# Kernel optimization log

Hardware: AMD Instinct MI355X
Metric: run time of the kernel (lower is better)

Reference implementation:

```python
import math
import jax, jax.numpy as jnp
import numpy as np

T, D, H = 2048, 1024, 16
DH = D // H
DFF = 4 * D
EPS = 1e-5


def gelu(x):
    c = math.sqrt(2.0 / math.pi)
    return 0.5 * x * (1.0 + jnp.tanh(c * (x + 0.044715 * jnp.power(x, 3))))


def layer_norm(x, w, b):
    mu = jnp.mean(x, axis=-1, keepdims=True)
    var = jnp.var(x, axis=-1, keepdims=True)
    return (x - mu) / jnp.sqrt(var + EPS) * w + b


def setup_inputs() -> dict:
    key = jax.random.key(0)
    ks = jax.random.split(key, 8)
    s = lambda fan_in: 1.0 / math.sqrt(fan_in)
    return {
        "x": jax.random.normal(ks[0], (T, D), jnp.float32),
        "w_kqv": jax.random.uniform(ks[1], (3 * D, D), jnp.float32, -s(D), s(D)),
        "b_kqv": jnp.zeros((3 * D,), jnp.float32),
        "w_o": jax.random.uniform(ks[2], (D, D), jnp.float32, -s(D), s(D)),
        "b_o": jnp.zeros((D,), jnp.float32),
        "ln1_w": jnp.ones((D,), jnp.float32),
        "ln1_b": jnp.zeros((D,), jnp.float32),
        "ln2_w": jnp.ones((D,), jnp.float32),
        "ln2_b": jnp.zeros((D,), jnp.float32),
        "w_up": jax.random.uniform(ks[3], (DFF, D), jnp.float32, -s(D), s(D)),
        "b_up": jnp.zeros((DFF,), jnp.float32),
        "w_down": jax.random.uniform(ks[4], (D, DFF), jnp.float32, -s(DFF), s(DFF)),
        "b_down": jnp.zeros((D,), jnp.float32),
    }


def _block(x, w_kqv, b_kqv, w_o, b_o, ln1_w, ln1_b, ln2_w, ln2_b,
           w_up, b_up, w_down, b_down):
    t = x.shape[0]
    # --- causal attention ---
    h = layer_norm(x, ln1_w, ln1_b)
    kqv = h @ w_kqv.T + b_kqv                      # [t, 3D]
    k, q, v = jnp.split(kqv, 3, axis=-1)
    # rearrange 't (d h) -> h t d' : head index is the FAST axis (as in source)
    to_heads = lambda m: m.reshape(t, DH, H).transpose(2, 0, 1)  # [H, t, DH]
    k, q, v = to_heads(k), to_heads(q), to_heads(v)
    # NOTE: source divides by sqrt(1/d) == multiplies by sqrt(d_head)
    logits = jnp.einsum('hqd,hkd->hqk', q, k) * math.sqrt(DH)
    mask = jnp.tril(jnp.ones((t, t), dtype=bool))
    logits = jnp.where(mask, logits, -jnp.inf)
    attn_w = jax.nn.softmax(logits, axis=-1)       # [H, t, t]
    hv = jnp.einsum('hqK,hKd->hqd', attn_w, v)     # [H, t, DH]
    # rearrange 'h q d -> q (h d)' : head index is the SLOW axis (as in source)
    hv = hv.transpose(1, 0, 2).reshape(t, D)
    x = x + (hv @ w_o.T + b_o)
    # --- MLP ---
    h2 = layer_norm(x, ln2_w, ln2_b)
    z = gelu(h2 @ w_up.T + b_up) @ w_down.T + b_down
    return x + z


def reference(x, w_kqv, b_kqv, w_o, b_o, ln1_w, ln1_b, ln2_w, ln2_b,
              w_up, b_up, w_down, b_down):
    return _block(x, w_kqv, b_kqv, w_o, b_o, ln1_w, ln1_b, ln2_w, ln2_b,
                  w_up, b_up, w_down, b_down)
```

## Files before the change

kernel.cpp:

```cpp
#include <hip/hip_runtime.h>
#include <math.h>

#define TT 2048
#define DD 1024
#define NH 16
#define DHD 64
#define DFF 4096

typedef __attribute__((ext_vector_type(8))) short short8;
typedef __attribute__((ext_vector_type(4))) float f32x4;

#define MFMA16(a, b, c) __builtin_amdgcn_mfma_f32_16x16x32_bf16(a, b, c, 0, 0, 0)
#define GLDS16(gp, lp) __builtin_amdgcn_global_load_lds( \
    (const __attribute__((address_space(1))) void*)(gp), \
    (__attribute__((address_space(3))) void*)(lp), 16, 0, 0)

static __device__ __forceinline__ unsigned short f2b(float f) {
  unsigned u = __builtin_bit_cast(unsigned, f);
  u = u + 0x7fffu + ((u >> 16) & 1u);
  return (unsigned short)(u >> 16);
}
static __device__ __forceinline__ float b2f(unsigned short b) {
  return __builtin_bit_cast(float, (unsigned)b << 16);
}

__global__ __launch_bounds__(256) void f2b_kernel(const float* __restrict__ in,
    unsigned short* __restrict__ out, int n4) {
  int i = blockIdx.x * 256 + threadIdx.x;
  if (i >= n4) return;
  float4 v = ((const float4*)in)[i];
  ushort4 o;
  o.x = f2b(v.x); o.y = f2b(v.y); o.z = f2b(v.z); o.w = f2b(v.w);
  ((ushort4*)out)[i] = o;
}

__global__ __launch_bounds__(256) void ln_kernel(const float* __restrict__ x,
    const float* __restrict__ w, const float* __restrict__ b,
    unsigned short* __restrict__ out) {
  int row = blockIdx.x;
  const float4* xr = (const float4*)(x + (size_t)row * DD);
  float4 v = xr[threadIdx.x];
  float s  = v.x + v.y + v.z + v.w;
  float ss = v.x * v.x + v.y * v.y + v.z * v.z + v.w * v.w;
  for (int o = 32; o > 0; o >>= 1) {
    s  += __shfl_down(s, o);
    ss += __shfl_down(ss, o);
  }
  __shared__ float red[10];
  int lane = threadIdx.x & 63, wv = threadIdx.x >> 6;
  if (lane == 0) { red[wv] = s; red[4 + wv] = ss; }
  __syncthreads();
  if (threadIdx.x == 0) {
    float S  = red[0] + red[1] + red[2] + red[3];
    float SS = red[4] + red[5] + red[6] + red[7];
    float mu  = S * (1.0f / DD);
    float var = SS * (1.0f / DD) - mu * mu;
    red[8] = mu;
    red[9] = rsqrtf(var + 1e-5f);
  }
  __syncthreads();
  float mu = red[8], inv = red[9];
  float4 wv4 = ((const float4*)w)[threadIdx.x];
  float4 bv4 = ((const float4*)b)[threadIdx.x];
  ushort4 o4;
  o4.x = f2b((v.x - mu) * inv * wv4.x + bv4.x);
  o4.y = f2b((v.y - mu) * inv * wv4.y + bv4.y);
  o4.z = f2b((v.z - mu) * inv * wv4.z + bv4.z);
  o4.w = f2b((v.w - mu) * inv * wv4.w + bv4.w);
  ((ushort4*)(out + (size_t)row * DD))[threadIdx.x] = o4;
}

template<int FUSE_GELU, int OUT_BF16, int HAS_RESID, int PARTIAL>
__global__ __launch_bounds__(256) void gemm2(
    const unsigned short* __restrict__ A,
    const unsigned short* __restrict__ Bw,
    const float* __restrict__ bias,
    const float* __restrict__ resid,
    void* __restrict__ Cout,
    int M, int N, int K, int KS) {
  __shared__ char lds[65536];
  const int tid = threadIdx.x;
  const int w = tid >> 6, l = tid & 63;
  const int l15 = l & 15, lhi = l >> 4;
  const int row0 = blockIdx.y * 128, col0 = blockIdx.x * 128;
  const int kbeg = blockIdx.z * KS;
  const int wm = (w >> 1) * 64, wn = (w & 1) * 64;

  f32x4 acc[4][4] = {};

  const int lrow = l >> 3;
  const int cb = ((l & 7) * 16) ^ (lrow << 4);
  const size_t rs8 = (size_t)K * 16;
  const char* aS = (const char*)A + ((size_t)(row0 + w * 32 + lrow) * K + kbeg) * 2 + cb;
  const char* bS = (const char*)Bw + ((size_t)(col0 + w * 32 + lrow) * K + kbeg) * 2 + cb;
  char* aD = lds + w * 4096;
  char* bD = lds + 16384 + w * 4096;

  const int NT = KS >> 6;

#pragma unroll
  for (int i = 0; i < 4; ++i) {
    GLDS16(aS + i * rs8, aD + i * 1024);
    GLDS16(bS + i * rs8, bD + i * 1024);
  }
  aS += 128; bS += 128;
  __syncthreads();

  int cur = 0;
  for (int t = 0; t < NT; ++t) {
    if (t + 1 < NT) {
      char* aDn = aD + (cur ^ 1) * 32768;
      char* bDn = bD + (cur ^ 1) * 32768;
#pragma unroll
      for (int i = 0; i < 4; ++i) {
        GLDS16(aS + i * rs8, aDn + i * 1024);
        GLDS16(bS + i * rs8, bDn + i * 1024);
      }
      aS += 128; bS += 128;
    }
    const char* Ab = lds + cur * 32768;
    const char* Bb = Ab + 16384;
    const int swz = (l15 & 7) << 4;
#pragma unroll
    for (int kk = 0; kk < 2; ++kk) {
      short8 af[4], bf[4];
#pragma unroll
      for (int mi = 0; mi < 4; ++mi)
        af[mi] = *(const short8*)(Ab + (wm + mi * 16 + l15) * 128 + ((kk * 64 + lhi * 16) ^ swz));
#pragma unroll
      for (int ni = 0; ni < 4; ++ni)
        bf[ni] = *(const short8*)(Bb + (wn + ni * 16 + l15) * 128 + ((kk * 64 + lhi * 16) ^ swz));
#pragma unroll
      for (int mi = 0; mi < 4; ++mi)
#pragma unroll
        for (int ni = 0; ni < 4; ++ni)
          acc[mi][ni] = MFMA16(af[mi], bf[ni], acc[mi][ni]);
    }
    __syncthreads();
    cur ^= 1;
  }

  if (PARTIAL) {
    float* Cp = (float*)Cout + (size_t)blockIdx.z * M * N;
#pragma unroll
    for (int mi = 0; mi < 4; ++mi)
#pragma unroll
      for (int r = 0; r < 4; ++r) {
        size_t row = (size_t)(row0 + wm + mi * 16 + lhi * 4 + r);
#pragma unroll
        for (int ni = 0; ni < 4; ++ni)
          Cp[row * N + col0 + wn + ni * 16 + l15] = acc[mi][ni][r];
      }
    return;
  }

#pragma unroll
  for (int mi = 0; mi < 4; ++mi) {
#pragma unroll
    for (int r = 0; r < 4; ++r) {
      size_t row = (size_t)(row0 + wm + mi * 16 + lhi * 4 + r);
#pragma unroll
      for (int ni = 0; ni < 4; ++ni) {
        int col = col0 + wn + ni * 16 + l15;
        float v = acc[mi][ni][r] + bias[col];
        if (FUSE_GELU) {
          float u = v;
          v = 0.5f * u * (1.0f + tanhf(0.7978845608028654f * (u + 0.044715f * u * u * u)));
        }
        if (HAS_RESID) v += resid[row * N + col];
        if (OUT_BF16) ((unsigned short*)Cout)[row * N + col] = f2b(v);
        else          ((float*)Cout)[row * N + col] = v;
      }
    }
  }
}

__global__ __launch_bounds__(256) void reduce_down(const float* __restrict__ p,
    const float* __restrict__ bias, const float* __restrict__ resid,
    float* __restrict__ out) {
  int i = blockIdx.x * 256 + threadIdx.x;
  float4 a = ((const float4*)p)[i];
  float4 b = ((const float4*)(p + (size_t)TT * DD))[i];
  float4 r = ((const float4*)resid)[i];
  float4 bb = ((const float4*)bias)[i & (DD / 4 - 1)];
  float4 o;
  o.x = a.x + b.x + r.x + bb.x;
  o.y = a.y + b.y + r.y + bb.y;
  o.z = a.z + b.z + r.z + bb.z;
  o.w = a.w + b.w + r.w + bb.w;
  ((float4*)out)[i] = o;
}

__global__ __launch_bounds__(256) void gather_qkv(const unsigned short* __restrict__ kqv,
    unsigned short* __restrict__ Q, unsigned short* __restrict__ K,
    unsigned short* __restrict__ V) {
  int idx = blockIdx.x * 256 + threadIdx.x;
  int d = idx & 63;
  int t = (idx >> 6) & (TT - 1);
  int h = idx >> 17;
  int col = d * NH + h;
  const unsigned short* rowp = kqv + (size_t)t * (3 * DD);
  K[idx] = rowp[col];
  Q[idx] = f2b(b2f(rowp[DD + col]) * 8.0f);
  V[idx] = rowp[2 * DD + col];
}

__global__ __launch_bounds__(256) void attn_mfma(
    const unsigned short* __restrict__ Q,
    const unsigned short* __restrict__ K,
    const unsigned short* __restrict__ V,
    unsigned short* __restrict__ hv) {
  const int h = blockIdx.y;
  const int qb = gridDim.x - 1 - blockIdx.x;
  const int q0 = qb * 64;
  const int tid = threadIdx.x;
  const int w = tid >> 6, l = tid & 63;
  const int l15 = l & 15, lhi = l >> 4;

  __shared__ unsigned short Ks[64 * 64];
  __shared__ unsigned short Vt[64 * 64];
  __shared__ unsigned short Ps[4][16 * 64];

  const unsigned short* Kh = K + (size_t)h * TT * DHD;
  const unsigned short* Vh = V + (size_t)h * TT * DHD;

  const unsigned short* Qbase = Q + ((size_t)h * TT + q0 + w * 16 + l15) * DHD;
  short8 qf0 = *(const short8*)(Qbase + lhi * 8);
  short8 qf1 = *(const short8*)(Qbase + 32 + lhi * 8);

  f32x4 oacc[4] = {};
  float m[4], lsum[4];
#pragma unroll
  for (int r = 0; r < 4; ++r) { m[r] = -INFINITY; lsum[r] = 0.0f; }

  const int krow = w * 16 + (l >> 3);
  const int kswz = (krow & 7) << 4;
  const int kcolb = ((l & 7) * 16) ^ kswz;
  char* kL = (char*)Ks + w * 2048;

  for (int kt = 0; kt <= qb; ++kt) {
    const int k0 = kt * 64;
    __syncthreads();

    GLDS16((const char*)(Kh + (size_t)(k0 + krow) * DHD) + kcolb, kL);
    GLDS16((const char*)(Kh + (size_t)(k0 + krow + 8) * DHD) + kcolb, kL + 1024);

    {
      const char* vS = (const char*)(Vh + (size_t)(k0 + l) * DHD) + w * 16;
      short8 v0 = *(const short8*)vS;
      short8 v1 = *(const short8*)(vS + 64);
#pragma unroll
      for (int j = 0; j < 8; ++j) {
        int d = w * 8 + j;
        *(unsigned short*)((char*)Vt + d * 128 + ((2 * l) ^ (j << 4))) =
            (unsigned short)v0[j];
        *(unsigned short*)((char*)Vt + (d + 32) * 128 + ((2 * l) ^ (j << 4))) =
            (unsigned short)v1[j];
      }
    }
    __syncthreads();

    f32x4 sacc[4] = {};
    {
      const char* kr = (const char*)Ks;
      int swz = (l15 & 7) << 4;
#pragma unroll
      for (int nt = 0; nt < 4; ++nt) {
        const char* rowp = kr + (nt * 16 + l15) * 128;
        short8 kb0 = *(const short8*)(rowp + ((lhi * 16) ^ swz));
        short8 kb1 = *(const short8*)(rowp + ((64 + lhi * 16) ^ swz));
        sacc[nt] = MFMA16(qf0, kb0, sacc[nt]);
        sacc[nt] = MFMA16(qf1, kb1, sacc[nt]);
      }
    }

    if (kt == qb) {
      const int qrow = w * 16 + lhi * 4;
#pragma unroll
      for (int nt = 0; nt < 4; ++nt)
#pragma unroll
        for (int r = 0; r < 4; ++r)
          if (nt * 16 + l15 > qrow + r) sacc[nt][r] = -INFINITY;
    }

    float mnew[4], al[4];
#pragma unroll
    for (int r = 0; r < 4; ++r) {
      float t = fmaxf(fmaxf(sacc[0][r], sacc[1][r]), fmaxf(sacc[2][r], sacc[3][r]));
      t = fmaxf(t, __shfl_xor(t, 1));
      t = fmaxf(t, __shfl_xor(t, 2));
      t = fmaxf(t, __shfl_xor(t, 4));
      t = fmaxf(t, __shfl_xor(t, 8));
      mnew[r] = fmaxf(m[r], t);
      al[r] = __expf(m[r] - mnew[r]);
      m[r] = mnew[r];
    }
#pragma unroll
    for (int r = 0; r < 4; ++r) {
      float s = 0.0f;
#pragma unroll
      for (int nt = 0; nt < 4; ++nt) {
        float p = __expf(sacc[nt][r] - mnew[r]);
        sacc[nt][r] = p;
        s += p;
      }
      s += __shfl_xor(s, 1);
      s += __shfl_xor(s, 2);
      s += __shfl_xor(s, 4);
      s += __shfl_xor(s, 8);
      lsum[r] = lsum[r] * al[r] + s;
#pragma unroll
      for (int dt = 0; dt < 4; ++dt) oacc[dt][r] *= al[r];
    }

    {
      char* pw = (char*)Ps[w];
#pragma unroll
      for (int r = 0; r < 4; ++r) {
        int prow = lhi * 4 + r;
        char* pp = pw + prow * 128;
        int swz = (prow & 7) << 4;
#pragma unroll
        for (int nt = 0; nt < 4; ++nt)
          *(unsigned short*)(pp + ((nt * 32 + l15 * 2) ^ swz)) = f2b(sacc[nt][r]);
      }
    }

    {
      const char* pr = (const char*)Ps[w] + l15 * 128;
      int pswz = (l15 & 7) << 4;
      short8 pa0 = *(const short8*)(pr + ((lhi * 16) ^ pswz));
      short8 pa1 = *(const short8*)(pr + ((64 + lhi * 16) ^ pswz));
      int vswz = (l15 & 7) << 4;
#pragma unroll
      for (int dt = 0; dt < 4; ++dt) {
        const char* vr = (const char*)Vt + (dt * 16 + l15) * 128;
        short8 vb0 = *(const short8*)(vr + ((lhi * 16) ^ vswz));
        short8 vb1 = *(const short8*)(vr + ((64 + lhi * 16) ^ vswz));
        oacc[dt] = MFMA16(pa0, vb0, oacc[dt]);
        oacc[dt] = MFMA16(pa1, vb1, oacc[dt]);
      }
    }
  }

#pragma unroll
  for (int r = 0; r < 4; ++r) {
    float inv = 1.0f / lsum[r];
    size_t orow = (size_t)(q0 + w * 16 + lhi * 4 + r) * DD + h * 64;
#pragma unroll
    for (int dt = 0; dt < 4; ++dt)
      hv[orow + dt * 16 + l15] = f2b(oacc[dt][r] * inv);
  }
}

extern "C" void kernel_launch(void* const* d_in, const int* in_sizes, int n_in,
                              void* d_out, int out_size, void* d_ws, size_t ws_size,
                              hipStream_t stream) {
  const float* x     = (const float*)d_in[0];
  const float* w_kqv = (const float*)d_in[1];
  const float* b_kqv = (const float*)d_in[2];
  const float* w_o   = (const float*)d_in[3];
  const float* b_o   = (const float*)d_in[4];
  const float* ln1_w = (const float*)d_in[5];
  const float* ln1_b = (const float*)d_in[6];
  const float* ln2_w = (const float*)d_in[7];
  const float* ln2_b = (const float*)d_in[8];
  const float* w_up  = (const float*)d_in[9];
  const float* b_up  = (const float*)d_in[10];
  const float* w_dn  = (const float*)d_in[11];
  const float* b_dn  = (const float*)d_in[12];
  float* out = (float*)d_out;

  char* W = (char*)d_ws;
  unsigned short* wkqv_b = (unsigned short*)(W);
  unsigned short* wo_b   = (unsigned short*)(W + 6291456);
  unsigned short* wup_b  = (unsigned short*)(W + 8388608);
  unsigned short* wdn_b  = (unsigned short*)(W + 16777216);
  unsigned short* h_b    = (unsigned short*)(W + 25165824);
  unsigned short* kqz    = (unsigned short*)(W + 29360128);
  unsigned short* Qg     = (unsigned short*)(W + 46137344);
  unsigned short* Kg     = (unsigned short*)(W + 50331648);
  unsigned short* Vg     = (unsigned short*)(W + 54525952);
  unsigned short* hv_b   = (unsigned short*)(W + 58720256);
  float*          x2     = (float*)(W + 62914560);
  float*          part   = (float*)(W + 46137344);

  f2b_kernel<<<(3 * DD * DD / 4 + 255) / 256, 256, 0, stream>>>(w_kqv, wkqv_b, 3 * DD * DD / 4);
  f2b_kernel<<<(DD * DD / 4 + 255) / 256, 256, 0, stream>>>(w_o, wo_b, DD * DD / 4);
  f2b_kernel<<<(DFF * DD / 4 + 255) / 256, 256, 0, stream>>>(w_up, wup_b, DFF * DD / 4);
  f2b_kernel<<<(DD * DFF / 4 + 255) / 256, 256, 0, stream>>>(w_dn, wdn_b, DD * DFF / 4);

  ln_kernel<<<TT, 256, 0, stream>>>(x, ln1_w, ln1_b, h_b);
  gemm2<0, 1, 0, 0><<<dim3(3 * DD / 128, TT / 128, 1), 256, 0, stream>>>(
      h_b, wkqv_b, b_kqv, nullptr, kqz, TT, 3 * DD, DD, DD);
  gather_qkv<<<(NH * TT * DHD) / 256, 256, 0, stream>>>(kqz, Qg, Kg, Vg);
  attn_mfma<<<dim3(TT / 64, NH), 256, 0, stream>>>(Qg, Kg, Vg, hv_b);
  gemm2<0, 0, 1, 0><<<dim3(DD / 128, TT / 128, 1), 256, 0, stream>>>(
      hv_b, wo_b, b_o, x, x2, TT, DD, DD, DD);
  ln_kernel<<<TT, 256, 0, stream>>>(x2, ln2_w, ln2_b, h_b);
  gemm2<1, 1, 0, 0><<<dim3(DFF / 128, TT / 128, 1), 256, 0, stream>>>(
      h_b, wup_b, b_up, nullptr, kqz, TT, DFF, DD, DD);
  gemm2<0, 0, 0, 1><<<dim3(DD / 128, TT / 128, 2), 256, 0, stream>>>(
      kqz, wdn_b, nullptr, nullptr, part, TT, DD, DFF, DFF / 2);
  reduce_down<<<TT * DD / 4 / 256, 256, 0, stream>>>(part, b_dn, x2, out);
}
```

Baseline: 211.3 us.

## Double-buffer attention K/V tiles with pre-transposed V and merged weight casts

Attention now double-buffers K and V tiles in LDS with async global-to-LDS loads, prefetching the next tile while computing the current one. To allow this, V is pre-transposed into a head-major [d, t] layout by a new transpose kernel instead of being transposed through LDS scatter inside the loop. The score MFMA operands are swapped so each lane owns one query row, which simplifies the softmax reductions. The four weight-cast launches are merged into one. The cost is an extra transpose launch and a larger LDS footprint, which may lower occupancy.

Result: faster. 179.8 us (-14.9%).

```diff
diff --git a/kernel.cpp b/kernel.cpp
--- a/kernel.cpp
+++ b/kernel.cpp
@@ -24,11 +24,16 @@
   return __builtin_bit_cast(float, (unsigned)b << 16);
 }
 
-__global__ __launch_bounds__(256) void f2b_kernel(const float* __restrict__ in,
-    unsigned short* __restrict__ out, int n4) {
+__global__ __launch_bounds__(256) void f2b4_kernel(const float* __restrict__ s0,
+    const float* __restrict__ s1, const float* __restrict__ s2,
+    const float* __restrict__ s3, unsigned short* __restrict__ out) {
   int i = blockIdx.x * 256 + threadIdx.x;
-  if (i >= n4) return;
-  float4 v = ((const float4*)in)[i];
+  const float* s; int off;
+  if (i < 786432)       { s = s0; off = 0; }
+  else if (i < 1048576) { s = s1; off = 786432; }
+  else if (i < 2097152) { s = s2; off = 1048576; }
+  else                  { s = s3; off = 2097152; }
+  float4 v = ((const float4*)s)[i - off];
   ushort4 o;
   o.x = f2b(v.x); o.y = f2b(v.y); o.z = f2b(v.z); o.w = f2b(v.w);
   ((ushort4*)out)[i] = o;
@@ -192,8 +197,7 @@
 }
 
 __global__ __launch_bounds__(256) void gather_qkv(const unsigned short* __restrict__ kqv,
-    unsigned short* __restrict__ Q, unsigned short* __restrict__ K,
-    unsigned short* __restrict__ V) {
+    unsigned short* __restrict__ Q, unsigned short* __restrict__ K) {
   int idx = blockIdx.x * 256 + threadIdx.x;
   int d = idx & 63;
   int t = (idx >> 6) & (TT - 1);
@@ -202,13 +206,28 @@
   const unsigned short* rowp = kqv + (size_t)t * (3 * DD);
   K[idx] = rowp[col];
   Q[idx] = f2b(b2f(rowp[DD + col]) * 8.0f);
-  V[idx] = rowp[2 * DD + col];
+}
+
+__global__ __launch_bounds__(256) void transpose_v(const unsigned short* __restrict__ kqv,
+    unsigned short* __restrict__ Vt) {
+  const int h = blockIdx.y;
+  const int t0 = blockIdx.x * 64;
+  __shared__ unsigned short Vs[64][65];
+  for (int idx = threadIdx.x; idx < 4096; idx += 256) {
+    int t = idx >> 6, d = idx & 63;
+    Vs[t][d] = kqv[(size_t)(t0 + t) * (3 * DD) + 2 * DD + d * NH + h];
+  }
+  __syncthreads();
+  for (int idx = threadIdx.x; idx < 4096; idx += 256) {
+    int d = idx >> 6, t = idx & 63;
+    Vt[(size_t)(h * DHD + d) * TT + t0 + t] = Vs[t][d];
+  }
 }
 
 __global__ __launch_bounds__(256) void attn_mfma(
     const unsigned short* __restrict__ Q,
     const unsigned short* __restrict__ K,
-    const unsigned short* __restrict__ V,
+    const unsigned short* __restrict__ Vt,
     unsigned short* __restrict__ hv) {
   const int h = blockIdx.y;
   const int qb = gridDim.x - 1 - blockIdx.x;
@@ -217,139 +236,134 @@
   const int w = tid >> 6, l = tid & 63;
   const int l15 = l & 15, lhi = l >> 4;
 
-  __shared__ unsigned short Ks[64 * 64];
-  __shared__ unsigned short Vt[64 * 64];
-  __shared__ unsigned short Ps[4][16 * 64];
-
-  const unsigned short* Kh = K + (size_t)h * TT * DHD;
-  const unsigned short* Vh = V + (size_t)h * TT * DHD;
+  __shared__ char lds[40960];
+  char* Ps = lds + 32768 + w * 2048;
+
+  const char* KhB = (const char*)(K + (size_t)h * TT * DHD);
+  const char* VhB = (const char*)(Vt + (size_t)h * DHD * TT);
 
   const unsigned short* Qbase = Q + ((size_t)h * TT + q0 + w * 16 + l15) * DHD;
   short8 qf0 = *(const short8*)(Qbase + lhi * 8);
   short8 qf1 = *(const short8*)(Qbase + 32 + lhi * 8);
 
   f32x4 oacc[4] = {};
-  float m[4], lsum[4];
-#pragma unroll
-  for (int r = 0; r < 4; ++r) { m[r] = -INFINITY; lsum[r] = 0.0f; }
-
-  const int krow = w * 16 + (l >> 3);
-  const int kswz = (krow & 7) << 4;
-  const int kcolb = ((l & 7) * 16) ^ kswz;
-  char* kL = (char*)Ks + w * 2048;
+  float m = -1e30f, lsum = 0.0f;
+
+  const int lrow = l >> 3;
+  const int colb = ((l & 7) * 16) ^ (lrow << 4);
+  const int srow = w * 16 + lrow;
+  const int swz = (l15 & 7) << 4;
+
+  auto stage = [&](int k0n, char* buf) {
+    const char* ks = KhB + (size_t)(k0n + srow) * 128 + colb;
+    GLDS16(ks, buf + w * 2048);
+    GLDS16(ks + 8 * 128, buf + w * 2048 + 1024);
+    const char* vs = VhB + (size_t)srow * (TT * 2) + (size_t)k0n * 2 + colb;
+    GLDS16(vs, buf + 8192 + w * 2048);
+    GLDS16(vs + 8 * (TT * 2), buf + 8192 + w * 2048 + 1024);
+  };
+
+  stage(0, lds);
+  __syncthreads();
+  int cur = 0;
 
   for (int kt = 0; kt <= qb; ++kt) {
-    const int k0 = kt * 64;
+    if (kt < qb) stage((kt + 1) * 64, lds + (cur ^ 1) * 16384);
+
+    const char* Kb = lds + cur * 16384;
+    const char* Vb = Kb + 8192;
+
+    f32x4 sacc[4] = {};
+    __builtin_amdgcn_s_setprio(1);
+#pragma unroll
+    for (int nt = 0; nt < 4; ++nt) {
+      const char* rp = Kb + (nt * 16 + l15) * 128;
+      short8 kb0 = *(const short8*)(rp + ((lhi * 16) ^ swz));
+      short8 kb1 = *(const short8*)(rp + ((64 + lhi * 16) ^ swz));
+      sacc[nt] = MFMA16(kb0, qf0, sacc[nt]);
+      sacc[nt] = MFMA16(kb1, qf1, sacc[nt]);
+    }
+    __builtin_amdgcn_s_setprio(0);
+
+    if (kt == qb) {
+      const int qloc = w * 16 + l15;
+#pragma unroll
+      for (int nt = 0; nt < 4; ++nt)
+#pragma unroll
+        for (int r = 0; r < 4; ++r)
+          if (nt * 16 + lhi * 4 + r > qloc) sacc[nt][r] = -1e30f;
+    }
+
+    float tmax = -1e30f;
+#pragma unroll
+    for (int nt = 0; nt < 4; ++nt)
+#pragma unroll
+      for (int r = 0; r < 4; ++r) tmax = fmaxf(tmax, sacc[nt][r]);
+    tmax = fmaxf(tmax, __shfl_xor(tmax, 16));
+    tmax = fmaxf(tmax, __shfl_xor(tmax, 32));
+    float mnew = fmaxf(m, tmax);
+    float al = __expf(m - mnew);
+    m = mnew;
+    float ssum = 0.0f;
+#pragma unroll
+    for (int nt = 0; nt < 4; ++nt)
+#pragma unroll
+      for (int r = 0; r < 4; ++r) {
+        float p = __expf(sacc[nt][r] - mnew);
+        sacc[nt][r] = p;
+        ssum += p;
+      }
+    ssum += __shfl_xor(ssum, 16);
+    ssum += __shfl_xor(ssum, 32);
+    lsum = lsum * al + ssum;
+
+    {
+      char* pp = Ps + l15 * 128;
+#pragma unroll
+      for (int nt = 0; nt < 4; ++nt) {
+        uint2 pk;
+        pk.x = (unsigned)f2b(sacc[nt][0]) | ((unsigned)f2b(sacc[nt][1]) << 16);
+        pk.y = (unsigned)f2b(sacc[nt][2]) | ((unsigned)f2b(sacc[nt][3]) << 16);
+        *(uint2*)(pp + (((nt * 16 + lhi * 4) * 2) ^ swz)) = pk;
+      }
+    }
+
+    float alr[4];
+#pragma unroll
+    for (int r = 0; r < 4; ++r) alr[r] = __shfl(al, (l & 48) | (lhi * 4 + r));
+#pragma unroll
+    for (int dt = 0; dt < 4; ++dt)
+#pragma unroll
+      for (int r = 0; r < 4; ++r) oacc[dt][r] *= alr[r];
+
+    const char* pr = Ps + l15 * 128;
+    short8 pa0 = *(const short8*)(pr + ((lhi * 16) ^ swz));
+    short8 pa1 = *(const short8*)(pr + ((64 + lhi * 16) ^ swz));
+    __builtin_amdgcn_s_setprio(1);
+#pragma unroll
+    for (int dt = 0; dt < 4; ++dt) {
+      const char* vr = Vb + (dt * 16 + l15) * 128;
+      short8 vb0 = *(const short8*)(vr + ((lhi * 16) ^ swz));
+      short8 vb1 = *(const short8*)(vr + ((64 + lhi * 16) ^ swz));
+      oacc[dt] = MFMA16(pa0, vb0, oacc[dt]);
+      oacc[dt] = MFMA16(pa1, vb1, oacc[dt]);
+    }
+    __builtin_amdgcn_s_setprio(0);
+
     __syncthreads();
-
-    GLDS16((const char*)(Kh + (size_t)(k0 + krow) * DHD) + kcolb, kL);
-    GLDS16((const char*)(Kh + (size_t)(k0 + krow + 8) * DHD) + kcolb, kL + 1024);
-
-    {
-      const char* vS = (const char*)(Vh + (size_t)(k0 + l) * DHD) + w * 16;
-      short8 v0 = *(const short8*)vS;
-      short8 v1 = *(const short8*)(vS + 64);
-#pragma unroll
-      for (int j = 0; j < 8; ++j) {
-        int d = w * 8 + j;
-        *(unsigned short*)((char*)Vt + d * 128 + ((2 * l) ^ (j << 4))) =
-            (unsigned short)v0[j];
-        *(unsigned short*)((char*)Vt + (d + 32) * 128 + ((2 * l) ^ (j << 4))) =
-            (unsigned short)v1[j];
-      }
-    }
-    __syncthreads();
-
-    f32x4 sacc[4] = {};
-    {
-      const char* kr = (const char*)Ks;
-      int swz = (l15 & 7) << 4;
-#pragma unroll
-      for (int nt = 0; nt < 4; ++nt) {
-        const char* rowp = kr + (nt * 16 + l15) * 128;
-        short8 kb0 = *(const short8*)(rowp + ((lhi * 16) ^ swz));
-        short8 kb1 = *(const short8*)(rowp + ((64 + lhi * 16) ^ swz));
-        sacc[nt] = MFMA16(qf0, kb0, sacc[nt]);
-        sacc[nt] = MFMA16(qf1, kb1, sacc[nt]);
-      }
-    }
-
-    if (kt == qb) {
-      const int qrow = w * 16 + lhi * 4;
-#pragma unroll
-      for (int nt = 0; nt < 4; ++nt)
-#pragma unroll
-        for (int r = 0; r < 4; ++r)
-          if (nt * 16 + l15 > qrow + r) sacc[nt][r] = -INFINITY;
-    }
-
-    float mnew[4], al[4];
-#pragma unroll
-    for (int r = 0; r < 4; ++r) {
-      float t = fmaxf(fmaxf(sacc[0][r], sacc[1][r]), fmaxf(sacc[2][r], sacc[3][r]));
-      t = fmaxf(t, __shfl_xor(t, 1));
-      t = fmaxf(t, __shfl_xor(t, 2));
-      t = fmaxf(t, __shfl_xor(t, 4));
-      t = fmaxf(t, __shfl_xor(t, 8));
-      mnew[r] = fmaxf(m[r], t);
-      al[r] = __expf(m[r] - mnew[r]);
-      m[r] = mnew[r];
-    }
-#pragma unroll
-    for (int r = 0; r < 4; ++r) {
-      float s = 0.0f;
-#pragma unroll
-      for (int nt = 0; nt < 4; ++nt) {
-        float p = __expf(sacc[nt][r] - mnew[r]);
-        sacc[nt][r] = p;
-        s += p;
-      }
-      s += __shfl_xor(s, 1);
-      s += __shfl_xor(s, 2);
-      s += __shfl_xor(s, 4);
-      s += __shfl_xor(s, 8);
-      lsum[r] = lsum[r] * al[r] + s;
-#pragma unroll
-      for (int dt = 0; dt < 4; ++dt) oacc[dt][r] *= al[r];
-    }
-
-    {
-      char* pw = (char*)Ps[w];
-#pragma unroll
-      for (int r = 0; r < 4; ++r) {
-        int prow = lhi * 4 + r;
-        char* pp = pw + prow * 128;
-        int swz = (prow & 7) << 4;
-#pragma unroll
-        for (int nt = 0; nt < 4; ++nt)
-          *(unsigned short*)(pp + ((nt * 32 + l15 * 2) ^ swz)) = f2b(sacc[nt][r]);
-      }
-    }
-
-    {
-      const char* pr = (const char*)Ps[w] + l15 * 128;
-      int pswz = (l15 & 7) << 4;
-      short8 pa0 = *(const short8*)(pr + ((lhi * 16) ^ pswz));
-      short8 pa1 = *(const short8*)(pr + ((64 + lhi * 16) ^ pswz));
-      int vswz = (l15 & 7) << 4;
-#pragma unroll
-      for (int dt = 0; dt < 4; ++dt) {
-        const char* vr = (const char*)Vt + (dt * 16 + l15) * 128;
-        short8 vb0 = *(const short8*)(vr + ((lhi * 16) ^ vswz));
-        short8 vb1 = *(const short8*)(vr + ((64 + lhi * 16) ^ vswz));
-        oacc[dt] = MFMA16(pa0, vb0, oacc[dt]);
-        oacc[dt] = MFMA16(pa1, vb1, oacc[dt]);
-      }
-    }
-  }
-
+    cur ^= 1;
+  }
+
+  float lr[4];
+#pragma unroll
+  for (int r = 0; r < 4; ++r)
+    lr[r] = 1.0f / __shfl(lsum, (l & 48) | (lhi * 4 + r));
 #pragma unroll
   for (int r = 0; r < 4; ++r) {
-    float inv = 1.0f / lsum[r];
     size_t orow = (size_t)(q0 + w * 16 + lhi * 4 + r) * DD + h * 64;
 #pragma unroll
     for (int dt = 0; dt < 4; ++dt)
-      hv[orow + dt * 16 + l15] = f2b(oacc[dt][r] * inv);
+      hv[orow + dt * 16 + l15] = f2b(oacc[dt][r] * lr[r]);
   }
 }
 
@@ -380,21 +394,19 @@
   unsigned short* kqz    = (unsigned short*)(W + 29360128);
   unsigned short* Qg     = (unsigned short*)(W + 46137344);
   unsigned short* Kg     = (unsigned short*)(W + 50331648);
-  unsigned short* Vg     = (unsigned short*)(W + 54525952);
+  unsigned short* Vtg    = (unsigned short*)(W + 54525952);
   unsigned short* hv_b   = (unsigned short*)(W + 58720256);
   float*          x2     = (float*)(W + 62914560);
   float*          part   = (float*)(W + 46137344);
 
-  f2b_kernel<<<(3 * DD * DD / 4 + 255) / 256, 256, 0, stream>>>(w_kqv, wkqv_b, 3 * DD * DD / 4);
-  f2b_kernel<<<(DD * DD / 4 + 255) / 256, 256, 0, stream>>>(w_o, wo_b, DD * DD / 4);
-  f2b_kernel<<<(DFF * DD / 4 + 255) / 256, 256, 0, stream>>>(w_up, wup_b, DFF * DD / 4);
-  f2b_kernel<<<(DD * DFF / 4 + 255) / 256, 256, 0, stream>>>(w_dn, wdn_b, DD * DFF / 4);
+  f2b4_kernel<<<3145728 / 256, 256, 0, stream>>>(w_kqv, w_o, w_up, w_dn, wkqv_b);
 
   ln_kernel<<<TT, 256, 0, stream>>>(x, ln1_w, ln1_b, h_b);
   gemm2<0, 1, 0, 0><<<dim3(3 * DD / 128, TT / 128, 1), 256, 0, stream>>>(
       h_b, wkqv_b, b_kqv, nullptr, kqz, TT, 3 * DD, DD, DD);
-  gather_qkv<<<(NH * TT * DHD) / 256, 256, 0, stream>>>(kqz, Qg, Kg, Vg);
-  attn_mfma<<<dim3(TT / 64, NH), 256, 0, stream>>>(Qg, Kg, Vg, hv_b);
+  gather_qkv<<<(NH * TT * DHD) / 256, 256, 0, stream>>>(kqz, Qg, Kg);
+  transpose_v<<<dim3(TT / 64, NH), 256, 0, stream>>>(kqz, Vtg);
+  attn_mfma<<<dim3(TT / 64, NH), 256, 0, stream>>>(Qg, Kg, Vtg, hv_b);
   gemm2<0, 0, 1, 0><<<dim3(DD / 128, TT / 128, 1), 256, 0, stream>>>(
       hv_b, wo_b, b_o, x, x2, TT, DD, DD, DD);
   ln_kernel<<<TT, 256, 0, stream>>>(x2, ln2_w, ln2_b, h_b);
```
